# Kernel optimization log

Hardware: AMD Instinct MI355X
Metric: run time of the kernel (lower is better)

## Reference

```python
import jax, jax.numpy as jnp
import numpy as np

WS = 7          # window_size
NH = 8          # num_heads
EMB = 128       # embedding_dim
HD = EMB // NH  # head_dim
SCALE = HD ** -0.5
LN_EPS = 1e-5


def setup_inputs() -> dict:
    key = jax.random.key(0)
    ks = jax.random.split(key, 5)
    B, N, C = 64, 3136, EMB  # H = W = 56
    x = jax.random.normal(ks[0], (B, N, C), dtype=jnp.float32)
    ln_gamma = jnp.ones((C,), dtype=jnp.float32)
    ln_beta = jnp.zeros((C,), dtype=jnp.float32)
    w_qkv = jax.random.normal(ks[1], (C, 3 * C), dtype=jnp.float32) * (C ** -0.5)
    b_qkv = jax.random.normal(ks[2], (3 * C,), dtype=jnp.float32) * 0.02
    w_out = jax.random.normal(ks[3], (C, C), dtype=jnp.float32) * (C ** -0.5)
    b_out = jax.random.normal(ks[4], (C,), dtype=jnp.float32) * 0.02
    return {"x": x, "ln_gamma": ln_gamma, "ln_beta": ln_beta,
            "w_qkv": w_qkv, "b_qkv": b_qkv, "w_out": w_out, "b_out": b_out}


def reference(x, ln_gamma, ln_beta, w_qkv, b_qkv, w_out, b_out):
    B, N, C = x.shape
    H = int(np.sqrt(N))  # static
    Wd = H

    # LayerNorm over last dim
    mu = jnp.mean(x, axis=-1, keepdims=True)
    var = jnp.mean(jnp.square(x - mu), axis=-1, keepdims=True)
    xn = (x - mu) * jax.lax.rsqrt(var + LN_EPS) * ln_gamma + ln_beta

    # divide windows: [B,N,C] -> [B*nWh*nWw, WS*WS, C]
    nW = H // WS
    win = xn.reshape(B, nW, WS, nW, WS, C).transpose(0, 1, 3, 2, 4, 5)
    win = win.reshape(-1, WS * WS, C)

    # QKV projection
    qkv = win @ w_qkv + b_qkv                      # [nw, 49, 3C]
    qkv = qkv.reshape(-1, WS * WS, 3, NH, HD).transpose(2, 0, 3, 1, 4)
    q, k, v = qkv[0], qkv[1], qkv[2]               # [nw, NH, 49, HD]

    scores = jnp.einsum('whqd,whkd->whqk', q, k) * SCALE
    probs = jax.nn.softmax(scores, axis=-1)
    attn = jnp.einsum('whqk,whkd->whqd', probs, v) # [nw, NH, 49, HD]
    attn = attn.transpose(0, 2, 1, 3).reshape(-1, WS * WS, C)

    out = attn @ w_out + b_out                     # [nw, 49, C]

    # merge windows -> [B, H, W, C]
    out = out.reshape(B, nW, nW, WS, WS, C).transpose(0, 1, 3, 2, 4, 5)
    return out.reshape(B, H, Wd, C)
```

## Files before the change

### kernel.cpp

```cpp
#include <hip/hip_runtime.h>

typedef float floatx4 __attribute__((ext_vector_type(4)));
typedef __bf16 bf16t;
typedef __bf16 bf16x8 __attribute__((ext_vector_type(8)));
typedef __bf16 bf16x4 __attribute__((ext_vector_type(4)));
typedef unsigned short u16t;
typedef unsigned int u32t;

static __device__ __forceinline__ u16t f2bf(float f) {
  return __builtin_bit_cast(u16t, (__bf16)f);
}
static __device__ __forceinline__ float bf2f(u16t h) {
  return __uint_as_float((u32t)h << 16);
}

#define MFMA(A, B, C) __builtin_amdgcn_mfma_f32_16x16x32_bf16((A), (B), (C), 0, 0, 0)

__global__ void pack_weights_kernel(const float* __restrict__ wqkv,
                                    const float* __restrict__ wout,
                                    u16t* __restrict__ wq_p,
                                    u16t* __restrict__ wo_p) {
  int g = blockIdx.x * blockDim.x + threadIdx.x;
  int l = g & 63;
  int s = (g >> 6) & 3;
  int n = g >> 8;
  int cl = l & 15;
  if (n < 24) {
    int kbase = 32 * s + ((l >> 4) * 8);
    int col = 16 * n + cl;
    u16t* dst = wq_p + g * 8;
#pragma unroll
    for (int j = 0; j < 8; ++j) dst[j] = f2bf(wqkv[(kbase + j) * 384 + col]);
  } else {
    int col = 16 * (n - 24) + cl;
    u16t* dst = wo_p + (g - 24 * 256) * 8;
    int rbase = 32 * s + 4 * (l >> 4);
#pragma unroll
    for (int j = 0; j < 8; ++j)
      dst[j] = f2bf(wout[(rbase + 16 * (j >> 2) + (j & 3)) * 128 + col]);
  }
}

__global__ __launch_bounds__(256, 4) void win_attn_kernel(
    const float* __restrict__ x, const float* __restrict__ gamma,
    const float* __restrict__ beta, const u16t* __restrict__ wq_p,
    const float* __restrict__ bqkv, const u16t* __restrict__ wo_p,
    const float* __restrict__ bout, float* __restrict__ out) {
  __shared__ u16t xnK[64][136];
  __shared__ u16t xv[9216];
  __shared__ u16t qs[64][40];

  const int tid = threadIdx.x;
  const int lane = tid & 63;
  const int w = tid >> 6;
  const int llo = lane & 15;
  const int lhi = lane >> 4;

  const int wi = blockIdx.x;
  const int bimg = wi >> 6;
  const int widx = wi & 63;
  const int nwh = widx >> 3;
  const int nww = widx & 7;
  const int base_off = (((bimg * 56) + nwh * 7) * 56 + nww * 7) * 128;
  const float* xbase = x + base_off;

  for (int i = tid; i < 15 * 64; i += 256) {
    int r = 49 + (i >> 6), c = (i & 63) << 1;
    *(u32t*)&xnK[r][c] = 0;
    *(u32t*)&xv[r * 136 + c] = 0;
  }

  {
    const float g0 = gamma[2 * lane], g1 = gamma[2 * lane + 1];
    const float b0 = beta[2 * lane], b1 = beta[2 * lane + 1];
    for (int t = w; t < 49; t += 4) {
      int wr = t / 7, wc = t - wr * 7;
      const float* row = xbase + (wr * 56 + wc) * 128;
      float2 v = *(const float2*)(row + 2 * lane);
      float sm = v.x + v.y;
      float sq = v.x * v.x + v.y * v.y;
#pragma unroll
      for (int m = 1; m < 64; m <<= 1) {
        sm += __shfl_xor(sm, m);
        sq += __shfl_xor(sq, m);
      }
      float mean = sm * (1.f / 128.f);
      float var = sq * (1.f / 128.f) - mean * mean;
      float rs = rsqrtf(var + 1e-5f);
      float y0 = (v.x - mean) * rs * g0 + b0;
      float y1 = (v.y - mean) * rs * g1 + b1;
      u16t h0 = f2bf(y0), h1 = f2bf(y1);
      u16t l0 = f2bf(y0 - bf2f(h0)), l1 = f2bf(y1 - bf2f(h1));
      *(u32t*)&xnK[t][2 * lane] = (u32t)h0 | ((u32t)h1 << 16);
      *(u32t*)&xv[t * 136 + 2 * lane] = (u32t)l0 | ((u32t)l1 << 16);
    }
  }
  __syncthreads();

  const int rowA = 16 * w + llo;
  const int rowC = 16 * w + lhi * 4;
  const floatx4 z4 = {0.f, 0.f, 0.f, 0.f};

  bf16x8 a_hi[4], a_lo[4];
#pragma unroll
  for (int s = 0; s < 4; ++s) {
    a_hi[s] = *(const bf16x8*)&xnK[rowA][s * 32 + lhi * 8];
    a_lo[s] = *(const bf16x8*)&xv[rowA * 136 + s * 32 + lhi * 8];
  }
  __syncthreads();

#pragma unroll 2
  for (int h = 0; h < 8; ++h) {
    const u16t* pwk = wq_p + (((8 + h) * 4) * 64 + lane) * 8;
    const u16t* pwv = wq_p + (((16 + h) * 4) * 64 + lane) * 8;
    floatx4 ak = z4, av = z4;
#pragma unroll
    for (int s = 0; s < 4; ++s) {
      bf16x8 bk = *(const bf16x8*)(pwk + s * 512);
      bf16x8 bv = *(const bf16x8*)(pwv + s * 512);
      ak = MFMA(bk, a_hi[s], ak);
      ak = MFMA(bk, a_lo[s], ak);
      av = MFMA(a_hi[s], bv, av);
      av = MFMA(a_lo[s], bv, av);
    }
    float4 bk4 = *(const float4*)(bqkv + 128 + h * 16 + 4 * lhi);
    ushort4 kk;
    kk.x = f2bf(ak[0] + bk4.x);
    kk.y = f2bf(ak[1] + bk4.y);
    kk.z = f2bf(ak[2] + bk4.z);
    kk.w = f2bf(ak[3] + bk4.w);
    *(ushort4*)&xnK[16 * w + llo][h * 16 + 4 * lhi] = kk;
    float bv_ = bqkv[256 + h * 16 + llo];
    ushort4 vv;
    vv.x = f2bf(av[0] + bv_);
    vv.y = f2bf(av[1] + bv_);
    vv.z = f2bf(av[2] + bv_);
    vv.w = f2bf(av[3] + bv_);
    *(ushort4*)&xv[(h * 16 + llo) * 72 + rowC] = vv;
  }

  {
    floatx4 aq = z4;
#pragma unroll
    for (int s = 0; s < 4; ++s) {
      bf16x8 bq0 = *(const bf16x8*)(wq_p + (s * 64 + lane) * 8);
      aq = MFMA(bq0, a_hi[s], aq);
    }
    float4 bq4 = *(const float4*)(bqkv + 4 * lhi);
    ushort4 qhv, qlv;
    float q0 = aq[0] + bq4.x, q1 = aq[1] + bq4.y;
    float q2 = aq[2] + bq4.z, q3 = aq[3] + bq4.w;
    qhv.x = f2bf(q0); qhv.y = f2bf(q1); qhv.z = f2bf(q2); qhv.w = f2bf(q3);
    qlv.x = f2bf(q0 - bf2f(qhv.x));
    qlv.y = f2bf(q1 - bf2f(qhv.y));
    qlv.z = f2bf(q2 - bf2f(qhv.z));
    qlv.w = f2bf(q3 - bf2f(qhv.w));
    *(ushort4*)&qs[16 * w + llo][4 * lhi] = qhv;
    *(ushort4*)&qs[16 * w + llo][16 + 4 * lhi] = qlv;
  }
  __syncthreads();

  bf16x8 kb[4];
  bf16x4 v00, v01, v10, v11;
  {
    const int bcol = (lhi & 1) * 8;
#pragma unroll
    for (int n = 0; n < 4; ++n)
      kb[n] = *(const bf16x8*)&xnK[16 * n + llo][bcol];
    const int vrow = llo * 72;
    v00 = *(const bf16x4*)&xv[vrow + 4 * lhi];
    v01 = *(const bf16x4*)&xv[vrow + 16 + 4 * lhi];
    v10 = *(const bf16x4*)&xv[vrow + 32 + 4 * lhi];
    v11 = *(const bf16x4*)&xv[vrow + 48 + 4 * lhi];
  }

  const float SEXP = 0.25f * 1.44269504088896340736f;
  floatx4 oc[8];
#pragma unroll
  for (int n = 0; n < 8; ++n) oc[n] = z4;

#pragma unroll 1
  for (int p4 = 0; p4 < 4; ++p4) {
    bf16x8 atf;
#pragma unroll
    for (int hp = 0; hp < 2; ++hp) {
      const int h = 2 * p4 + hp;
      bf16x8 bqn0, bqn1, bqn2, bqn3;
      if (h < 7) {
        const u16t* pq = wq_p + (((h + 1) * 4) * 64 + lane) * 8;
        bqn0 = *(const bf16x8*)(pq);
        bqn1 = *(const bf16x8*)(pq + 512);
        bqn2 = *(const bf16x8*)(pq + 1024);
        bqn3 = *(const bf16x8*)(pq + 1536);
      }
      __asm__ volatile("s_waitcnt lgkmcnt(0)" ::: "memory");

      bf16x8 aqf = *(const bf16x8*)&qs[16 * w + llo][8 * lhi];
      floatx4 sc[4];
#pragma unroll
      for (int n = 0; n < 4; ++n) sc[n] = MFMA(kb[n], aqf, z4);

      if (h < 7) {
        floatx4 aq = MFMA(bqn0, a_hi[0], z4);
        aq = MFMA(bqn1, a_hi[1], aq);
        aq = MFMA(bqn2, a_hi[2], aq);
        aq = MFMA(bqn3, a_hi[3], aq);
        float4 bq4 = *(const float4*)(bqkv + (h + 1) * 16 + 4 * lhi);
        float q0 = aq[0] + bq4.x, q1 = aq[1] + bq4.y;
        float q2 = aq[2] + bq4.z, q3 = aq[3] + bq4.w;
        ushort4 qhv, qlv;
        qhv.x = f2bf(q0); qhv.y = f2bf(q1); qhv.z = f2bf(q2); qhv.w = f2bf(q3);
        qlv.x = f2bf(q0 - bf2f(qhv.x));
        qlv.y = f2bf(q1 - bf2f(qhv.y));
        qlv.z = f2bf(q2 - bf2f(qhv.z));
        qlv.w = f2bf(q3 - bf2f(qhv.w));
        *(ushort4*)&qs[16 * w + llo][4 * lhi] = qhv;
        *(ushort4*)&qs[16 * w + llo][16 + 4 * lhi] = qlv;
      }

      float s0 = 0.f;
#pragma unroll
      for (int n = 0; n < 4; ++n) {
#pragma unroll
        for (int j = 0; j < 4; ++j) {
          float pe;
          if (n == 3)
            pe = (4 * lhi + j < 1) ? exp2f(sc[n][j] * SEXP) : 0.f;
          else
            pe = exp2f(sc[n][j] * SEXP);
          sc[n][j] = pe;
          s0 += pe;
        }
      }
      s0 += __shfl_xor(s0, 16);
      s0 += __shfl_xor(s0, 32);
      float rq = 1.f / s0;

      bf16x8 PB0, PB1;
#pragma unroll
      for (int j = 0; j < 4; ++j) {
        PB0[j] = (bf16t)sc[0][j];
        PB0[4 + j] = (bf16t)sc[1][j];
        PB1[j] = (bf16t)sc[2][j];
        PB1[4 + j] = (bf16t)sc[3][j];
      }
      bf16x8 V0 = __builtin_shufflevector(v00, v01, 0, 1, 2, 3, 4, 5, 6, 7);
      bf16x8 V1 = __builtin_shufflevector(v10, v11, 0, 1, 2, 3, 4, 5, 6, 7);
      floatx4 ao = MFMA(V0, PB0, z4);
      ao = MFMA(V1, PB1, ao);
      atf[4 * hp + 0] = (bf16t)(ao[0] * rq);
      atf[4 * hp + 1] = (bf16t)(ao[1] * rq);
      atf[4 * hp + 2] = (bf16t)(ao[2] * rq);
      atf[4 * hp + 3] = (bf16t)(ao[3] * rq);

      if (h < 7) {
        const int bcol = (h + 1) * 16 + (lhi & 1) * 8;
#pragma unroll
        for (int n = 0; n < 4; ++n)
          kb[n] = *(const bf16x8*)&xnK[16 * n + llo][bcol];
        const int vrow = ((h + 1) * 16 + llo) * 72;
        v00 = *(const bf16x4*)&xv[vrow + 4 * lhi];
        v01 = *(const bf16x4*)&xv[vrow + 16 + 4 * lhi];
        v10 = *(const bf16x4*)&xv[vrow + 32 + 4 * lhi];
        v11 = *(const bf16x4*)&xv[vrow + 48 + 4 * lhi];
      }
    }
#pragma unroll
    for (int n = 0; n < 8; ++n)
      oc[n] = MFMA(atf,
                   *(const bf16x8*)(wo_p + ((n * 4 + p4) * 64 + lane) * 8),
                   oc[n]);
  }

  float bo[8];
#pragma unroll
  for (int n = 0; n < 8; ++n) bo[n] = bout[16 * n + llo];
  float* obase = out + base_off;
#pragma unroll
  for (int r = 0; r < 4; ++r) {
    int t = rowC + r;
    if (t < 49) {
      int wr = t / 7, wc = t - wr * 7;
      float* orow = obase + (wr * 56 + wc) * 128;
#pragma unroll
      for (int n = 0; n < 8; ++n) orow[16 * n + llo] = oc[n][r] + bo[n];
    }
  }
}

extern "C" void kernel_launch(void* const* d_in, const int* in_sizes, int n_in,
                              void* d_out, int out_size, void* d_ws,
                              size_t ws_size, hipStream_t stream) {
  const float* x = (const float*)d_in[0];
  const float* ln_g = (const float*)d_in[1];
  const float* ln_b = (const float*)d_in[2];
  const float* w_qkv = (const float*)d_in[3];
  const float* b_qkv = (const float*)d_in[4];
  const float* w_out = (const float*)d_in[5];
  const float* b_out = (const float*)d_in[6];
  float* out = (float*)d_out;

  u16t* wq_p = (u16t*)d_ws;
  u16t* wo_p = wq_p + 24 * 256 * 8;

  hipLaunchKernelGGL(pack_weights_kernel, dim3(32), dim3(256), 0, stream,
                     w_qkv, w_out, wq_p, wo_p);
  hipLaunchKernelGGL(win_attn_kernel, dim3(4096), dim3(256), 0, stream, x,
                     ln_g, ln_b, wq_p, b_qkv, wo_p, b_out, out);
}
```

Baseline: 310.7 us.

## Keep Q fragments in registers and duplicate K halves instead of LDS staging

Removes the shared-memory Q staging buffer. The hi/lo bf16 split of Q is now built directly in the register layout the score MFMA consumes. The K operand is loaded as 4 elements and duplicated across both halves, so one MFMA computes q_hi·k + q_lo·k. The next head's K/V loads are issued earlier and the next Q projection moves after the PV product, which also drops the explicit lgkmcnt wait and some LDS traffic. This relies on a precise lane/fragment mapping and keeps more live registers.

```diff
diff --git a/kernel.cpp b/kernel.cpp
--- a/kernel.cpp
+++ b/kernel.cpp
@@ -48,7 +48,6 @@
     const float* __restrict__ bout, float* __restrict__ out) {
   __shared__ u16t xnK[64][136];
   __shared__ u16t xv[9216];
-  __shared__ u16t qs[64][40];
 
   const int tid = threadIdx.x;
   const int lane = tid & 63;
@@ -107,6 +106,10 @@
     a_hi[s] = *(const bf16x8*)&xnK[rowA][s * 32 + lhi * 8];
     a_lo[s] = *(const bf16x8*)&xv[rowA * 136 + s * 32 + lhi * 8];
   }
+  bf16x8 bqw[4];
+#pragma unroll
+  for (int s = 0; s < 4; ++s)
+    bqw[s] = *(const bf16x8*)(wq_p + (s * 64 + lane) * 8);
   __syncthreads();
 
 #pragma unroll 2
@@ -139,34 +142,29 @@
     *(ushort4*)&xv[(h * 16 + llo) * 72 + rowC] = vv;
   }
 
+  bf16x8 qf;
   {
     floatx4 aq = z4;
 #pragma unroll
-    for (int s = 0; s < 4; ++s) {
-      bf16x8 bq0 = *(const bf16x8*)(wq_p + (s * 64 + lane) * 8);
-      aq = MFMA(bq0, a_hi[s], aq);
-    }
+    for (int s = 0; s < 4; ++s) aq = MFMA(bqw[s], a_hi[s], aq);
     float4 bq4 = *(const float4*)(bqkv + 4 * lhi);
-    ushort4 qhv, qlv;
     float q0 = aq[0] + bq4.x, q1 = aq[1] + bq4.y;
     float q2 = aq[2] + bq4.z, q3 = aq[3] + bq4.w;
-    qhv.x = f2bf(q0); qhv.y = f2bf(q1); qhv.z = f2bf(q2); qhv.w = f2bf(q3);
-    qlv.x = f2bf(q0 - bf2f(qhv.x));
-    qlv.y = f2bf(q1 - bf2f(qhv.y));
-    qlv.z = f2bf(q2 - bf2f(qhv.z));
-    qlv.w = f2bf(q3 - bf2f(qhv.w));
-    *(ushort4*)&qs[16 * w + llo][4 * lhi] = qhv;
-    *(ushort4*)&qs[16 * w + llo][16 + 4 * lhi] = qlv;
+    qf[0] = (bf16t)q0; qf[1] = (bf16t)q1;
+    qf[2] = (bf16t)q2; qf[3] = (bf16t)q3;
+    qf[4] = (bf16t)(q0 - (float)qf[0]);
+    qf[5] = (bf16t)(q1 - (float)qf[1]);
+    qf[6] = (bf16t)(q2 - (float)qf[2]);
+    qf[7] = (bf16t)(q3 - (float)qf[3]);
   }
   __syncthreads();
 
-  bf16x8 kb[4];
+  bf16x4 kv4[4];
   bf16x4 v00, v01, v10, v11;
   {
-    const int bcol = (lhi & 1) * 8;
 #pragma unroll
     for (int n = 0; n < 4; ++n)
-      kb[n] = *(const bf16x8*)&xnK[16 * n + llo][bcol];
+      kv4[n] = *(const bf16x4*)&xnK[16 * n + llo][4 * lhi];
     const int vrow = llo * 72;
     v00 = *(const bf16x4*)&xv[vrow + 4 * lhi];
     v01 = *(const bf16x4*)&xv[vrow + 16 + 4 * lhi];
@@ -185,37 +183,31 @@
 #pragma unroll
     for (int hp = 0; hp < 2; ++hp) {
       const int h = 2 * p4 + hp;
-      bf16x8 bqn0, bqn1, bqn2, bqn3;
       if (h < 7) {
         const u16t* pq = wq_p + (((h + 1) * 4) * 64 + lane) * 8;
-        bqn0 = *(const bf16x8*)(pq);
-        bqn1 = *(const bf16x8*)(pq + 512);
-        bqn2 = *(const bf16x8*)(pq + 1024);
-        bqn3 = *(const bf16x8*)(pq + 1536);
-      }
-      __asm__ volatile("s_waitcnt lgkmcnt(0)" ::: "memory");
-
-      bf16x8 aqf = *(const bf16x8*)&qs[16 * w + llo][8 * lhi];
+#pragma unroll
+        for (int s = 0; s < 4; ++s) bqw[s] = *(const bf16x8*)(pq + s * 512);
+      }
+
       floatx4 sc[4];
 #pragma unroll
-      for (int n = 0; n < 4; ++n) sc[n] = MFMA(kb[n], aqf, z4);
-
+      for (int n = 0; n < 4; ++n) {
+        bf16x8 kbf =
+            __builtin_shufflevector(kv4[n], kv4[n], 0, 1, 2, 3, 0, 1, 2, 3);
+        sc[n] = MFMA(kbf, qf, z4);
+      }
+
+      bf16x4 nk[4], nv0, nv1, nv2, nv3;
       if (h < 7) {
-        floatx4 aq = MFMA(bqn0, a_hi[0], z4);
-        aq = MFMA(bqn1, a_hi[1], aq);
-        aq = MFMA(bqn2, a_hi[2], aq);
-        aq = MFMA(bqn3, a_hi[3], aq);
-        float4 bq4 = *(const float4*)(bqkv + (h + 1) * 16 + 4 * lhi);
-        float q0 = aq[0] + bq4.x, q1 = aq[1] + bq4.y;
-        float q2 = aq[2] + bq4.z, q3 = aq[3] + bq4.w;
-        ushort4 qhv, qlv;
-        qhv.x = f2bf(q0); qhv.y = f2bf(q1); qhv.z = f2bf(q2); qhv.w = f2bf(q3);
-        qlv.x = f2bf(q0 - bf2f(qhv.x));
-        qlv.y = f2bf(q1 - bf2f(qhv.y));
-        qlv.z = f2bf(q2 - bf2f(qhv.z));
-        qlv.w = f2bf(q3 - bf2f(qhv.w));
-        *(ushort4*)&qs[16 * w + llo][4 * lhi] = qhv;
-        *(ushort4*)&qs[16 * w + llo][16 + 4 * lhi] = qlv;
+        const int kcol = (h + 1) * 16 + 4 * lhi;
+#pragma unroll
+        for (int n = 0; n < 4; ++n)
+          nk[n] = *(const bf16x4*)&xnK[16 * n + llo][kcol];
+        const int vrow = ((h + 1) * 16 + llo) * 72;
+        nv0 = *(const bf16x4*)&xv[vrow + 4 * lhi];
+        nv1 = *(const bf16x4*)&xv[vrow + 16 + 4 * lhi];
+        nv2 = *(const bf16x4*)&xv[vrow + 32 + 4 * lhi];
+        nv3 = *(const bf16x4*)&xv[vrow + 48 + 4 * lhi];
       }
 
       float s0 = 0.f;
@@ -254,15 +246,21 @@
       atf[4 * hp + 3] = (bf16t)(ao[3] * rq);
 
       if (h < 7) {
-        const int bcol = (h + 1) * 16 + (lhi & 1) * 8;
-#pragma unroll
-        for (int n = 0; n < 4; ++n)
-          kb[n] = *(const bf16x8*)&xnK[16 * n + llo][bcol];
-        const int vrow = ((h + 1) * 16 + llo) * 72;
-        v00 = *(const bf16x4*)&xv[vrow + 4 * lhi];
-        v01 = *(const bf16x4*)&xv[vrow + 16 + 4 * lhi];
-        v10 = *(const bf16x4*)&xv[vrow + 32 + 4 * lhi];
-        v11 = *(const bf16x4*)&xv[vrow + 48 + 4 * lhi];
+        floatx4 aq = z4;
+#pragma unroll
+        for (int s = 0; s < 4; ++s) aq = MFMA(bqw[s], a_hi[s], aq);
+        float4 bq4 = *(const float4*)(bqkv + (h + 1) * 16 + 4 * lhi);
+        float q0 = aq[0] + bq4.x, q1 = aq[1] + bq4.y;
+        float q2 = aq[2] + bq4.z, q3 = aq[3] + bq4.w;
+        qf[0] = (bf16t)q0; qf[1] = (bf16t)q1;
+        qf[2] = (bf16t)q2; qf[3] = (bf16t)q3;
+        qf[4] = (bf16t)(q0 - (float)qf[0]);
+        qf[5] = (bf16t)(q1 - (float)qf[1]);
+        qf[6] = (bf16t)(q2 - (float)qf[2]);
+        qf[7] = (bf16t)(q3 - (float)qf[3]);
+#pragma unroll
+        for (int n = 0; n < 4; ++n) kv4[n] = nk[n];
+        v00 = nv0; v01 = nv1; v10 = nv2; v11 = nv3;
       }
     }
 #pragma unroll
```

New measurement: 331.7 us. 1.07x slower.
